# Kernel tuning notes

Hardware: AMD Instinct MI355X
Metric: run time of the kernel (lower is better)

Reference implementation:

```python
import jax, jax.numpy as jnp
import numpy as np
import math

_GELU_C = math.sqrt(2.0 / math.pi)

def gelu(x):
    # custom tanh-approx GELU from the torch module
    return 0.5 * x * (1.0 + jnp.tanh(_GELU_C * (x + 0.044715 * x ** 3)))

def setup_inputs() -> dict:
    key = jax.random.key(0)
    ks = jax.random.split(key, 6)
    N, D, B, npm = 16384, 128, 256, 64   # total nodes, dim, molecules, atoms/mol
    NF = 10000                            # N_fingerprints
    fingerprints = jax.random.randint(ks[0], (N,), 0, NF)
    seg = jnp.arange(N) // npm
    block = seg[:, None] == seg[None, :]  # block-diagonal structure of padded adjacency
    adjacency = jnp.where(block & (jax.random.uniform(ks[1], (N, N)) < 0.15), 1.0, 0.0).astype(jnp.float32)
    s = 1.0 / math.sqrt(D)
    embed = jax.random.normal(ks[2], (NF, D), jnp.float32)
    W_fp_w = jax.random.normal(ks[3], (3, D, D), jnp.float32) * s
    W_fp_b = jnp.zeros((3, D), jnp.float32)
    W_out_w = jax.random.normal(ks[4], (2, D, D), jnp.float32) * s
    W_out_b = jnp.zeros((2, D), jnp.float32)
    masks = jnp.ones((B, 1), jnp.float32)
    return {"fingerprints": fingerprints, "adjacency": adjacency, "embed": embed,
            "W_fp_w": W_fp_w, "W_fp_b": W_fp_b, "W_out_w": W_out_w, "W_out_b": W_out_b,
            "masks": masks, "nodes_per_mol": npm}

def reference(fingerprints, adjacency, embed, W_fp_w, W_fp_b, W_out_w, W_out_b, masks, nodes_per_mol):
    N = fingerprints.shape[0]
    B = masks.shape[0]
    seg = jnp.arange(N) // nodes_per_mol  # segment ids replacing torch.split python loop
    v = embed[fingerprints]               # [N, D] embedding lookup
    for l in range(W_fp_w.shape[0]):      # GNN hidden layers
        h = gelu(v @ W_fp_w[l].T + W_fp_b[l])
        h = h + adjacency @ h             # residual + block-diagonal message passing
        v = h / jnp.maximum(jnp.linalg.norm(h, axis=1, keepdims=True), 1e-12)  # F.normalize(h,2,1)
    mol = jax.ops.segment_sum(v, seg, num_segments=B)  # mode='sum' pooling -> [B, D]
    for l in range(W_out_w.shape[0]):     # W_output_ layers
        mol = gelu(mol @ W_out_w[l].T + W_out_b[l])
    return mol * masks
```

## Files before the change

### kernel.cpp

```cpp
#include <hip/hip_runtime.h>
#include <hip/hip_bf16.h>

#define D    128
#define NPM  64
#define NMOL 256
#define NTOT 16384
#define SK   136
#define ST   72
#define XPLANE 9216

typedef __attribute__((ext_vector_type(8))) short bf16x8;
typedef __attribute__((ext_vector_type(4))) float f32x4;

__device__ __forceinline__ unsigned short f2bf(float x){
    union { float f; unsigned u; } c; c.f = x;
    unsigned r = c.u + 0x7FFFu + ((c.u >> 16) & 1u);
    return (unsigned short)(r >> 16);
}
__device__ __forceinline__ float bf2f(unsigned short h){
    union { float f; unsigned u; } c; c.u = ((unsigned)h) << 16;
    return c.f;
}
__device__ __forceinline__ float gelu_f(float x){
    float z = 0.7978845608028654f * (x + 0.044715f * x * x * x);
    float e = __expf(2.0f * z);
    float t = 1.0f - 2.0f / (e + 1.0f);
    return 0.5f * x * (1.0f + t);
}

__global__ void prep_w_split(const float* __restrict__ W,
                             unsigned short* __restrict__ hi,
                             unsigned short* __restrict__ lo, int n){
    int i = blockIdx.x * blockDim.x + threadIdx.x;
    if (i < n){
        float x = W[i];
        unsigned short h = f2bf(x);
        hi[i] = h;
        lo[i] = f2bf(x - bf2f(h));
    }
}

__global__ __launch_bounds__(512)
void mgnn_kernel(const int*   __restrict__ fps,
                 const float* __restrict__ adjacency,
                 const float* __restrict__ embed,
                 const unsigned short* __restrict__ Whi,
                 const unsigned short* __restrict__ Wlo,
                 const float* __restrict__ Wfb,
                 const float* __restrict__ Wout,
                 const float* __restrict__ Wob,
                 const float* __restrict__ masks,
                 float* __restrict__ out)
{
    __shared__ __attribute__((aligned(16))) unsigned short sXhi[XPLANE];
    __shared__ __attribute__((aligned(16))) unsigned short sXlo[XPLANE];
    __shared__ __attribute__((aligned(16))) unsigned short sAdj[NPM * ST];
    __shared__ int   sFp[NPM];
    __shared__ float sSS[NPM * 2];
    __shared__ float sMolPart[4 * D];
    __shared__ __attribute__((aligned(16))) float sMolF[D];
    __shared__ __attribute__((aligned(16))) float sY[D];

    const int tid  = threadIdx.x;
    const int blk  = blockIdx.x;
    const int lane = tid & 63;
    const int wave = tid >> 6;
    const int l15  = lane & 15;
    const int q    = lane >> 4;
    const int mt   = wave & 3;
    const int nh   = wave >> 2;
    const int base = blk * NPM;

    if (tid < NPM) sFp[tid] = fps[base + tid];
    #pragma unroll
    for (int u = 0; u < 8; ++u){
        int idx = tid + 512 * u;
        int r = idx >> 6, c = idx & 63;
        float a = adjacency[(size_t)(base + r) * NTOT + (base + c)];
        sAdj[r * ST + c] = f2bf(a);
    }
    __syncthreads();

    #pragma unroll
    for (int u = 0; u < 16; ++u){
        int idx = tid + 512 * u;
        int r = idx >> 7, j = idx & 127;
        float v = embed[sFp[r] * D + j];
        unsigned short h = f2bf(v);
        sXhi[r * SK + j] = h;
        sXlo[r * SK + j] = f2bf(v - bf2f(h));
    }
    __syncthreads();

    const f32x4 zero4 = {0.f, 0.f, 0.f, 0.f};
    float vreg[4][4];

    for (int l = 0; l < 3; ++l){
        f32x4 acc[4] = {zero4, zero4, zero4, zero4};
        const int row_a = 16 * mt + l15;
        const unsigned short* WhiL = Whi + l * D * D;
        const unsigned short* WloL = Wlo + l * D * D;
        #pragma unroll
        for (int kt = 0; kt < 4; ++kt){
            int kb = kt * 32 + 8 * q;
            bf16x8 ahi = *(const bf16x8*)&sXhi[row_a * SK + kb];
            bf16x8 alo = *(const bf16x8*)&sXlo[row_a * SK + kb];
            #pragma unroll
            for (int tt = 0; tt < 4; ++tt){
                int n = 16 * (4 * nh + tt) + l15;
                bf16x8 bhi = *(const bf16x8*)&WhiL[n * D + kb];
                bf16x8 blo = *(const bf16x8*)&WloL[n * D + kb];
                acc[tt] = __builtin_amdgcn_mfma_f32_16x16x32_bf16(ahi, bhi, acc[tt], 0, 0, 0);
                acc[tt] = __builtin_amdgcn_mfma_f32_16x16x32_bf16(alo, bhi, acc[tt], 0, 0, 0);
                acc[tt] = __builtin_amdgcn_mfma_f32_16x16x32_bf16(ahi, blo, acc[tt], 0, 0, 0);
            }
        }
        __syncthreads();

        float hreg[4][4];
        #pragma unroll
        for (int tt = 0; tt < 4; ++tt){
            int j = 64 * nh + 16 * tt + l15;
            float bias = Wfb[l * D + j];
            #pragma unroll
            for (int reg = 0; reg < 4; ++reg){
                int i = 16 * mt + 4 * q + reg;
                float h = gelu_f(acc[tt][reg] + bias);
                hreg[tt][reg] = h;
                unsigned short hh = f2bf(h);
                sXhi[j * ST + i] = hh;
                sXlo[j * ST + i] = f2bf(h - bf2f(hh));
            }
        }
        __syncthreads();

        f32x4 racc[4] = {zero4, zero4, zero4, zero4};
        #pragma unroll
        for (int kt = 0; kt < 2; ++kt){
            int kb = kt * 32 + 8 * q;
            bf16x8 aadj = *(const bf16x8*)&sAdj[(16 * mt + l15) * ST + kb];
            #pragma unroll
            for (int tt = 0; tt < 4; ++tt){
                int n = 16 * (4 * nh + tt) + l15;
                bf16x8 bhi = *(const bf16x8*)&sXhi[n * ST + kb];
                bf16x8 blo = *(const bf16x8*)&sXlo[n * ST + kb];
                racc[tt] = __builtin_amdgcn_mfma_f32_16x16x32_bf16(aadj, bhi, racc[tt], 0, 0, 0);
                racc[tt] = __builtin_amdgcn_mfma_f32_16x16x32_bf16(aadj, blo, racc[tt], 0, 0, 0);
            }
        }

        float o[4][4];
        float p[4] = {0.f, 0.f, 0.f, 0.f};
        #pragma unroll
        for (int tt = 0; tt < 4; ++tt)
            #pragma unroll
            for (int reg = 0; reg < 4; ++reg){
                float v = hreg[tt][reg] + racc[tt][reg];
                o[tt][reg] = v;
                p[reg] += v * v;
            }
        #pragma unroll
        for (int d2 = 1; d2 <= 8; d2 <<= 1)
            #pragma unroll
            for (int reg = 0; reg < 4; ++reg)
                p[reg] += __shfl_xor(p[reg], d2);
        if (l15 == 0){
            #pragma unroll
            for (int reg = 0; reg < 4; ++reg)
                sSS[(16 * mt + 4 * q + reg) * 2 + nh] = p[reg];
        }
        __syncthreads();

        #pragma unroll
        for (int reg = 0; reg < 4; ++reg){
            int i = 16 * mt + 4 * q + reg;
            float ss = sSS[i * 2 + 0] + sSS[i * 2 + 1];
            float sc = 1.0f / fmaxf(sqrtf(ss), 1e-12f);
            #pragma unroll
            for (int tt = 0; tt < 4; ++tt)
                vreg[tt][reg] = o[tt][reg] * sc;
        }

        if (l < 2){
            #pragma unroll
            for (int tt = 0; tt < 4; ++tt){
                int j = 64 * nh + 16 * tt + l15;
                #pragma unroll
                for (int reg = 0; reg < 4; ++reg){
                    int i = 16 * mt + 4 * q + reg;
                    float v = vreg[tt][reg];
                    unsigned short h = f2bf(v);
                    sXhi[i * SK + j] = h;
                    sXlo[i * SK + j] = f2bf(v - bf2f(h));
                }
            }
            __syncthreads();
        }
    }

    float msum[4];
    #pragma unroll
    for (int tt = 0; tt < 4; ++tt){
        msum[tt] = vreg[tt][0] + vreg[tt][1] + vreg[tt][2] + vreg[tt][3];
        msum[tt] += __shfl_xor(msum[tt], 16);
        msum[tt] += __shfl_xor(msum[tt], 32);
    }
    if (q == 0){
        #pragma unroll
        for (int tt = 0; tt < 4; ++tt){
            int j = 64 * nh + 16 * tt + l15;
            sMolPart[mt * D + j] = msum[tt];
        }
    }
    __syncthreads();
    if (tid < D)
        sMolF[tid] = sMolPart[0 * D + tid] + sMolPart[1 * D + tid]
                   + sMolPart[2 * D + tid] + sMolPart[3 * D + tid];
    __syncthreads();

    if (tid < D){
        const float4* wr = (const float4*)&Wout[(0 * D + tid) * D];
        const float4* mv = (const float4*)sMolF;
        float s = 0.f;
        #pragma unroll
        for (int k = 0; k < 32; ++k){
            float4 w = wr[k], m = mv[k];
            s += w.x * m.x + w.y * m.y + w.z * m.z + w.w * m.w;
        }
        sY[tid] = gelu_f(s + Wob[tid]);
    }
    __syncthreads();
    if (tid < D){
        const float4* wr = (const float4*)&Wout[(1 * D + tid) * D];
        const float4* yv = (const float4*)sY;
        float s = 0.f;
        #pragma unroll
        for (int k = 0; k < 32; ++k){
            float4 w = wr[k], y = yv[k];
            s += w.x * y.x + w.y * y.y + w.z * y.z + w.w * y.w;
        }
        float z = gelu_f(s + Wob[D + tid]);
        out[blk * D + tid] = z * masks[blk];
    }
}

extern "C" void kernel_launch(void* const* d_in, const int* in_sizes, int n_in,
                              void* d_out, int out_size, void* d_ws, size_t ws_size,
                              hipStream_t stream) {
    const int*   fps = (const int*)  d_in[0];
    const float* adj = (const float*)d_in[1];
    const float* emb = (const float*)d_in[2];
    const float* Wfw = (const float*)d_in[3];
    const float* Wfb = (const float*)d_in[4];
    const float* Wow = (const float*)d_in[5];
    const float* Wob = (const float*)d_in[6];
    const float* msk = (const float*)d_in[7];

    unsigned short* Whi = (unsigned short*)d_ws;
    unsigned short* Wlo = Whi + 3 * D * D;
    const int nW = 3 * D * D;

    prep_w_split<<<(nW + 255) / 256, 256, 0, stream>>>(Wfw, Whi, Wlo, nW);
    mgnn_kernel<<<NMOL, 512, 0, stream>>>(fps, adj, emb, Whi, Wlo, Wfb,
                                          Wow, Wob, msk, (float*)d_out);
}
```

Before: 1.162 ms.

## Fuse weight hi/lo split into main kernel and stage weights in LDS

Removes the separate prep kernel that split the fp32 weights into bf16 hi/lo planes. Each block now converts the layer weights itself into padded shared-memory buffers and reloads the next layer's weights after the GELU stage. The GEMM B operands then come from LDS instead of global memory. In exchange every block redoes the conversion, LDS use grows by about 68KB, and the barrier structure now has to protect the weight buffers too.

```diff
diff --git a/kernel.cpp b/kernel.cpp
--- a/kernel.cpp
+++ b/kernel.cpp
@@ -7,6 +7,7 @@
 #define NTOT 16384
 #define SK   136
 #define ST   72
+#define SW   136
 #define XPLANE 9216
 
 typedef __attribute__((ext_vector_type(8))) short bf16x8;
@@ -28,24 +29,11 @@
     return 0.5f * x * (1.0f + t);
 }
 
-__global__ void prep_w_split(const float* __restrict__ W,
-                             unsigned short* __restrict__ hi,
-                             unsigned short* __restrict__ lo, int n){
-    int i = blockIdx.x * blockDim.x + threadIdx.x;
-    if (i < n){
-        float x = W[i];
-        unsigned short h = f2bf(x);
-        hi[i] = h;
-        lo[i] = f2bf(x - bf2f(h));
-    }
-}
-
 __global__ __launch_bounds__(512)
 void mgnn_kernel(const int*   __restrict__ fps,
                  const float* __restrict__ adjacency,
                  const float* __restrict__ embed,
-                 const unsigned short* __restrict__ Whi,
-                 const unsigned short* __restrict__ Wlo,
+                 const float* __restrict__ Wfw,
                  const float* __restrict__ Wfb,
                  const float* __restrict__ Wout,
                  const float* __restrict__ Wob,
@@ -54,6 +42,8 @@
 {
     __shared__ __attribute__((aligned(16))) unsigned short sXhi[XPLANE];
     __shared__ __attribute__((aligned(16))) unsigned short sXlo[XPLANE];
+    __shared__ __attribute__((aligned(16))) unsigned short sWhi[D * SW];
+    __shared__ __attribute__((aligned(16))) unsigned short sWlo[D * SW];
     __shared__ __attribute__((aligned(16))) unsigned short sAdj[NPM * ST];
     __shared__ int   sFp[NPM];
     __shared__ float sSS[NPM * 2];
@@ -79,6 +69,15 @@
         float a = adjacency[(size_t)(base + r) * NTOT + (base + c)];
         sAdj[r * ST + c] = f2bf(a);
     }
+    #pragma unroll
+    for (int u = 0; u < 32; ++u){
+        int idx = tid + 512 * u;
+        int n = idx >> 7, k = idx & 127;
+        float w = Wfw[idx];
+        unsigned short h = f2bf(w);
+        sWhi[n * SW + k] = h;
+        sWlo[n * SW + k] = f2bf(w - bf2f(h));
+    }
     __syncthreads();
 
     #pragma unroll
@@ -98,8 +97,6 @@
     for (int l = 0; l < 3; ++l){
         f32x4 acc[4] = {zero4, zero4, zero4, zero4};
         const int row_a = 16 * mt + l15;
-        const unsigned short* WhiL = Whi + l * D * D;
-        const unsigned short* WloL = Wlo + l * D * D;
         #pragma unroll
         for (int kt = 0; kt < 4; ++kt){
             int kb = kt * 32 + 8 * q;
@@ -108,8 +105,8 @@
             #pragma unroll
             for (int tt = 0; tt < 4; ++tt){
                 int n = 16 * (4 * nh + tt) + l15;
-                bf16x8 bhi = *(const bf16x8*)&WhiL[n * D + kb];
-                bf16x8 blo = *(const bf16x8*)&WloL[n * D + kb];
+                bf16x8 bhi = *(const bf16x8*)&sWhi[n * SW + kb];
+                bf16x8 blo = *(const bf16x8*)&sWlo[n * SW + kb];
                 acc[tt] = __builtin_amdgcn_mfma_f32_16x16x32_bf16(ahi, bhi, acc[tt], 0, 0, 0);
                 acc[tt] = __builtin_amdgcn_mfma_f32_16x16x32_bf16(alo, bhi, acc[tt], 0, 0, 0);
                 acc[tt] = __builtin_amdgcn_mfma_f32_16x16x32_bf16(ahi, blo, acc[tt], 0, 0, 0);
@@ -130,6 +127,18 @@
                 unsigned short hh = f2bf(h);
                 sXhi[j * ST + i] = hh;
                 sXlo[j * ST + i] = f2bf(h - bf2f(hh));
+            }
+        }
+        if (l < 2){
+            const float* Wl = Wfw + (l + 1) * D * D;
+            #pragma unroll
+            for (int u = 0; u < 32; ++u){
+                int idx = tid + 512 * u;
+                int n = idx >> 7, k = idx & 127;
+                float w = Wl[idx];
+                unsigned short h = f2bf(w);
+                sWhi[n * SW + k] = h;
+                sWlo[n * SW + k] = f2bf(w - bf2f(h));
             }
         }
         __syncthreads();
@@ -256,11 +265,6 @@
     const float* Wob = (const float*)d_in[6];
     const float* msk = (const float*)d_in[7];
 
-    unsigned short* Whi = (unsigned short*)d_ws;
-    unsigned short* Wlo = Whi + 3 * D * D;
-    const int nW = 3 * D * D;
-
-    prep_w_split<<<(nW + 255) / 256, 256, 0, stream>>>(Wfw, Whi, Wlo, nW);
-    mgnn_kernel<<<NMOL, 512, 0, stream>>>(fps, adj, emb, Whi, Wlo, Wfb,
+    mgnn_kernel<<<NMOL, 512, 0, stream>>>(fps, adj, emb, Wfw, Wfb,
                                           Wow, Wob, msk, (float*)d_out);
 }
```

New measurement: 1.159 ms. Within noise of the previous version (-0.3%).
